# Kernel tuning notes

Hardware: AMD Instinct MI355X
Metric: run time of the kernel (lower is better)

## Reference

```python
import jax, jax.numpy as jnp
import numpy as np

B, N, D_M, H, D_K, R, GRID = 2, 2048, 128, 8, 16, 4, 64


def setup_inputs() -> dict:
    key = jax.random.key(0)
    ks = jax.random.split(key, 12)
    z = jax.random.normal(ks[0], (B, N, D_M), dtype=jnp.float32)
    patch_token = jax.random.normal(ks[1], (B, 1, D_M), dtype=jnp.float32)
    positions = jax.random.randint(ks[2], (B, N, 2), 0, GRID, dtype=jnp.int32)
    alive_mask = (jax.random.uniform(ks[3], (B, N, 1)) > 0.1).astype(jnp.float32)
    s = 0.02
    Wq = jax.random.normal(ks[4], (D_M, H * D_K), dtype=jnp.float32) * s
    Wk = jax.random.normal(ks[5], (D_M, H * D_K), dtype=jnp.float32) * s
    Wv = jax.random.normal(ks[6], (D_M, H * D_K), dtype=jnp.float32) * s
    Wo = jax.random.normal(ks[7], (H * D_K, D_M), dtype=jnp.float32) * s
    bq = jnp.zeros((H * D_K,), jnp.float32)
    bk = jnp.zeros((H * D_K,), jnp.float32)
    bv = jnp.zeros((H * D_K,), jnp.float32)
    bo = jnp.zeros((D_M,), jnp.float32)
    rel_bias = jax.random.normal(ks[8], (H, 2 * R + 1, 2 * R + 1), dtype=jnp.float32) * s
    return {"z": z, "patch_token": patch_token, "positions": positions, "alive_mask": alive_mask,
            "Wq": Wq, "bq": bq, "Wk": Wk, "bk": bk, "Wv": Wv, "bv": bv, "Wo": Wo, "bo": bo,
            "rel_bias": rel_bias}


def reference(z, patch_token, positions, alive_mask, Wq, bq, Wk, bk, Wv, bv, Wo, bo, rel_bias):
    B_, N_, _ = z.shape
    H_ = rel_bias.shape[0]
    R_ = (rel_bias.shape[1] - 1) // 2
    dk = Wq.shape[1] // H_
    alive = alive_mask                                   # [B,N,1] float 0/1
    z_a = z * alive
    tokens = jnp.concatenate([z_a, patch_token], axis=1)  # [B,N+1,d_m]
    q = (z_a @ Wq + bq).reshape(B_, N_, H_, dk).transpose(0, 2, 1, 3)       # [B,H,N,dk]
    k = (tokens @ Wk + bk).reshape(B_, N_ + 1, H_, dk).transpose(0, 2, 1, 3)
    v = (tokens @ Wv + bv).reshape(B_, N_ + 1, H_, dk).transpose(0, 2, 1, 3)
    q = q * alive[:, None]                               # [B,1,N,1] broadcast
    logits = jnp.einsum('bhnd,bhmd->bhnm', q, k) / jnp.sqrt(jnp.float32(dk))  # [B,H,N,N+1]
    # Chebyshev mask (delta = pos_i - pos_j)
    delta = positions[:, :, None, :] - positions[:, None, :, :]               # [B,N,N,2]
    cheb = jnp.maximum(jnp.abs(delta[..., 0]), jnp.abs(delta[..., 1]))
    alive_j = alive[:, :, 0] > 0
    not_self = ~jnp.eye(N_, dtype=bool)
    allowed = (cheb <= R_) & alive_j[:, None, :] & not_self[None]
    mask_agents = jnp.where(allowed, 0.0, -1e9).astype(jnp.float32)           # [B,N,N]
    # Relative-position bias (torch uses delta_rel = pos_j - pos_i = -delta)
    dx = -delta[..., 0] + R_
    dy = -delta[..., 1] + R_
    valid = (dx >= 0) & (dx <= 2 * R_) & (dy >= 0) & (dy <= 2 * R_)
    flat = jnp.clip(dx, 0, 2 * R_) * (2 * R_ + 1) + jnp.clip(dy, 0, 2 * R_)   # [B,N,N] int
    table = rel_bias.reshape(H_, -1)
    rel = jnp.moveaxis(jnp.take(table, flat, axis=1), 0, 1)                   # [B,H,N,N]
    rel = rel * valid[:, None].astype(jnp.float32)
    add = mask_agents[:, None] + rel                                          # [B,H,N,N]
    logits = logits + jnp.pad(add, ((0, 0), (0, 0), (0, 0), (0, 1)))          # patch col: mask 0, no bias
    logits = jnp.where(alive[:, None] > 0, logits, -1e9)                      # dead queries
    attn = jax.nn.softmax(logits, axis=-1)
    out = jnp.einsum('bhnm,bhmd->bhnd', attn, v)
    out = out.transpose(0, 2, 1, 3).reshape(B_, N_, H_ * dk)
    out = (out @ Wo + bo) * alive
    return out
```

## Files before the change

kernel.cpp:

```cpp
#include <hip/hip_runtime.h>
#include <hip/hip_fp16.h>
#include <math.h>

#define BB 2
#define NN 2048
#define NP1 2049
#define DM 128
#define NH 8
#define DK 16
#define RWIN 4
#define GRID_W 64
#define QPB 8
#define CAND_PQ 160

__device__ __forceinline__ void unpack8(uint4 r, float* f) {
    float2 t;
    t = __half22float2(*(const __half2*)&r.x); f[0] = t.x; f[1] = t.y;
    t = __half22float2(*(const __half2*)&r.y); f[2] = t.x; f[3] = t.y;
    t = __half22float2(*(const __half2*)&r.z); f[4] = t.x; f[5] = t.y;
    t = __half22float2(*(const __half2*)&r.w); f[6] = t.x; f[7] = t.y;
}


#define QKV_ROWS 8

__global__ __launch_bounds__(384) void qkv_kernel(
    const float* __restrict__ z, const float* __restrict__ patch,
    const float* __restrict__ Wq, const float* __restrict__ bq,
    const float* __restrict__ Wk, const float* __restrict__ bk,
    const float* __restrict__ Wv, const float* __restrict__ bv,
    float* __restrict__ q, __half* __restrict__ k, __half* __restrict__ v) {
    __shared__ float zrow[QKV_ROWS][DM];
    const int tid = threadIdx.x;
    const int mat = tid >> 7;
    const int rem = tid & 127;
    const int cg = rem & 31;
    const int rs = rem >> 5;
    const int r0 = blockIdx.x * QKV_ROWS;
    const int NROWS = BB * NP1;

    if (tid < QKV_ROWS * DM / 4) {
        int r = tid >> 5, q4 = tid & 31;
        int row = r0 + r;
        float4 val = make_float4(0.f, 0.f, 0.f, 0.f);
        if (row < NROWS) {
            int b = row / NP1, ti = row % NP1;
            const float* src = (ti < NN) ? (z + ((size_t)b * NN + ti) * DM)
                                         : (patch + (size_t)b * DM);
            val = ((const float4*)src)[q4];
        }
        *((float4*)&zrow[r][q4 * 4]) = val;
    }
    __syncthreads();

    const float* W    = (mat == 0) ? Wq : (mat == 1) ? Wk : Wv;
    const float* bias = (mat == 0) ? bq : (mat == 1) ? bk : bv;

    float a0x = 0.f, a0y = 0.f, a0z = 0.f, a0w = 0.f;
    float a1x = 0.f, a1y = 0.f, a1z = 0.f, a1w = 0.f;
#pragma unroll 8
    for (int kk = 0; kk < DM; ++kk) {
        float4 w4 = *((const float4*)(W + kk * DM + cg * 4));
        float z0 = zrow[rs][kk];
        float z1 = zrow[rs + 4][kk];
        a0x = fmaf(z0, w4.x, a0x); a0y = fmaf(z0, w4.y, a0y);
        a0z = fmaf(z0, w4.z, a0z); a0w = fmaf(z0, w4.w, a0w);
        a1x = fmaf(z1, w4.x, a1x); a1y = fmaf(z1, w4.y, a1y);
        a1z = fmaf(z1, w4.z, a1z); a1w = fmaf(z1, w4.w, a1w);
    }
    float4 b4 = *((const float4*)(bias + cg * 4));
    float4 o0 = make_float4(a0x + b4.x, a0y + b4.y, a0z + b4.z, a0w + b4.w);
    float4 o1 = make_float4(a1x + b4.x, a1y + b4.y, a1z + b4.z, a1w + b4.w);

#pragma unroll
    for (int rr = 0; rr < 2; ++rr) {
        int row = r0 + rs + rr * 4;
        if (row >= NROWS) break;
        float4 val = rr ? o1 : o0;
        int b = row / NP1, ti = row % NP1;
        if (mat == 0) {
            if (ti < NN) ((float4*)(q + ((size_t)b * NN + ti) * DM))[cg] = val;
        } else {
            __half2 p0 = __floats2half2_rn(val.x, val.y);
            __half2 p1 = __floats2half2_rn(val.z, val.w);
            uint2 st;
            st.x = *(unsigned int*)&p0;
            st.y = *(unsigned int*)&p1;
            __half* dst = ((mat == 1) ? k : v) + ((size_t)b * NP1 + ti) * DM;
            ((uint2*)dst)[cg] = st;
        }
    }
}


__global__ __launch_bounds__(256) void attn_out_kernel(
    const float* __restrict__ q, const __half* __restrict__ k, const __half* __restrict__ v,
    const int* __restrict__ positions, const float* __restrict__ alive,
    const float* __restrict__ rel_bias, const float* __restrict__ Wo,
    const float* __restrict__ bo, float* __restrict__ out) {
    const int tid = threadIdx.x;
    const int qq = tid >> 5;
    const int lane = tid & 31;
    const int h = lane >> 2;
    const int s = lane & 3;
    const int r0 = blockIdx.x * QPB;
    const int b = r0 >> 11;
    const int bi = r0 + qq;

    __shared__ float sbias[NH * 81];
    __shared__ int   spx[QPB], spy[QPB];
    __shared__ float sal[QPB];
    __shared__ int   mcount[QPB];
    __shared__ int   cand[QPB][CAND_PQ];
    __shared__ float po[QPB * 4][DM + 1];
    __shared__ float pl[QPB * 4][NH + 1];
    __shared__ float srow[QPB][DM + 1];

    if (tid < QPB) {
        mcount[tid] = 0;
        int gbi = r0 + tid;
        spx[tid] = positions[gbi * 2 + 0];
        spy[tid] = positions[gbi * 2 + 1];
        sal[tid] = alive[gbi];
    }
    for (int t = tid; t < NH * 81; t += 256) sbias[t] = rel_bias[t];

    const __half* kb = k + (size_t)b * NP1 * DM;
    const __half* vb = v + (size_t)b * NP1 * DM;

    float qf[16];
    {
        const float4* qr = (const float4*)(q + (size_t)bi * DM + h * DK);
#pragma unroll
        for (int e = 0; e < 4; ++e) {
            float4 t4 = qr[e];
            qf[e * 4 + 0] = t4.x * 0.25f; qf[e * 4 + 1] = t4.y * 0.25f;
            qf[e * 4 + 2] = t4.z * 0.25f; qf[e * 4 + 3] = t4.w * 0.25f;
        }
    }

    __syncthreads();

    int qx[QPB], qy[QPB], qi[QPB];
    float qa[QPB];
#pragma unroll
    for (int u = 0; u < QPB; ++u) {
        qx[u] = spx[u]; qy[u] = spy[u]; qa[u] = sal[u];
        qi[u] = (r0 + u) & (NN - 1);
    }

    const int2* pb = (const int2*)(positions + (size_t)b * NN * 2);
    const float* ab = alive + (size_t)b * NN;
#pragma unroll
    for (int u = 0; u < NN / 256; ++u) {
        int j = u * 256 + tid;
        int2 pj = pb[j];
        float aj = ab[j];
        if (aj > 0.5f) {
            int packed = j | (pj.x << 16) | (pj.y << 24);
#pragma unroll
            for (int qn = 0; qn < QPB; ++qn) {
                int dx = pj.x - qx[qn]; dx = dx < 0 ? -dx : dx;
                int dy = pj.y - qy[qn]; dy = dy < 0 ? -dy : dy;
                int ch = dx > dy ? dx : dy;
                if (ch <= RWIN && j != qi[qn] && qa[qn] > 0.5f) {
                    int slot = atomicAdd(&mcount[qn], 1);
                    if (slot < CAND_PQ) cand[qn][slot] = packed;
                }
            }
        }
    }
    __syncthreads();
    int M = mcount[qq]; if (M > CAND_PQ) M = CAND_PQ;
    const int pix = qx[qq], piy = qy[qq];

    float l = 0.f;
    float o[16];
#pragma unroll
    for (int e = 0; e < 16; ++e) o[e] = 0.f;

    if (s == 0) {
        const uint4* kr = (const uint4*)(kb + (size_t)NN * DM + h * DK);
        uint4 ka = kr[0], kb4 = kr[1];
        const uint4* vr = (const uint4*)(vb + (size_t)NN * DM + h * DK);
        uint4 va = vr[0], vb4 = vr[1];
        float kf[16], vf[16];
        unpack8(ka, kf); unpack8(kb4, kf + 8);
        unpack8(va, vf); unpack8(vb4, vf + 8);
        float d = 0.f;
#pragma unroll
        for (int e = 0; e < 16; ++e) d = fmaf(qf[e], kf[e], d);
        float p = __expf(d);
        l += p;
#pragma unroll
        for (int e = 0; e < 16; ++e) o[e] = fmaf(p, vf[e], o[e]);
    }

    for (int t = s; t < M; t += 4) {
        int packed = cand[qq][t];
        int j = packed & 0xFFFF;
        const uint4* kr = (const uint4*)(kb + (size_t)j * DM + h * DK);
        uint4 ka = kr[0], kb4 = kr[1];
        const uint4* vr = (const uint4*)(vb + (size_t)j * DM + h * DK);
        uint4 va = vr[0], vb4 = vr[1];
        float kf[16], vf[16];
        unpack8(ka, kf); unpack8(kb4, kf + 8);
        unpack8(va, vf); unpack8(vb4, vf + 8);
        float d = 0.f;
#pragma unroll
        for (int e = 0; e < 16; ++e) d = fmaf(qf[e], kf[e], d);
        int pjx = (packed >> 16) & 0xFF;
        int pjy = (packed >> 24) & 0xFF;
        float bias = sbias[h * 81 + (pjx - pix + RWIN) * 9 + (pjy - piy + RWIN)];
        float p = __expf(d + bias);
        l += p;
#pragma unroll
        for (int e = 0; e < 16; ++e) o[e] = fmaf(p, vf[e], o[e]);
    }

    {
        const int prow = qq * 4 + s;
#pragma unroll
        for (int e = 0; e < 16; ++e) po[prow][h * DK + e] = o[e];
        pl[prow][h] = l;
    }
    __syncthreads();
    {
        const int c = tid & 127;
        const int g = tid >> 7;
        const int ch = c >> 4;
#pragma unroll
        for (int qn = 0; qn < 4; ++qn) {
            int qq2 = g * 4 + qn;
            float acc = 0.f, lh = 0.f;
#pragma unroll
            for (int ss = 0; ss < 4; ++ss) {
                acc += po[qq2 * 4 + ss][c];
                lh  += pl[qq2 * 4 + ss][ch];
            }
            srow[qq2][c] = acc / lh;
        }
    }
    __syncthreads();

    {
        const int oq = tid >> 5;
        const int c4 = lane;
        float ax = 0.f, ay = 0.f, az = 0.f, aw = 0.f;
#pragma unroll 8
        for (int kk = 0; kk < DM; ++kk) {
            float sv = srow[oq][kk];
            float4 w4 = *((const float4*)(Wo + kk * DM + c4 * 4));
            ax = fmaf(sv, w4.x, ax); ay = fmaf(sv, w4.y, ay);
            az = fmaf(sv, w4.z, az); aw = fmaf(sv, w4.w, aw);
        }
        float ga = sal[oq] > 0.5f ? 1.f : 0.f;
        float4 b4 = *((const float4*)(bo + c4 * 4));
        float4 r;
        r.x = (ax + b4.x) * ga; r.y = (ay + b4.y) * ga;
        r.z = (az + b4.z) * ga; r.w = (aw + b4.w) * ga;
        ((float4*)(out + (size_t)(r0 + oq) * DM))[c4] = r;
    }
}

extern "C" void kernel_launch(void* const* d_in, const int* in_sizes, int n_in,
                              void* d_out, int out_size, void* d_ws, size_t ws_size,
                              hipStream_t stream) {
    const float* z         = (const float*)d_in[0];
    const float* patch     = (const float*)d_in[1];
    const int*   positions = (const int*)d_in[2];
    const float* alive     = (const float*)d_in[3];
    const float* Wq        = (const float*)d_in[4];
    const float* bq        = (const float*)d_in[5];
    const float* Wk        = (const float*)d_in[6];
    const float* bk        = (const float*)d_in[7];
    const float* Wv        = (const float*)d_in[8];
    const float* bv        = (const float*)d_in[9];
    const float* Wo        = (const float*)d_in[10];
    const float* bo        = (const float*)d_in[11];
    const float* rel_bias  = (const float*)d_in[12];
    float* out = (float*)d_out;

    char* ws = (char*)d_ws;
    size_t off = 0;
    auto alloc = [&](size_t bytes) -> void* {
        void* p = ws + off;
        off += (bytes + 255) & ~(size_t)255;
        return p;
    };
    float*  q = (float*)alloc((size_t)BB * NN * DM * 4);
    __half* k = (__half*)alloc((size_t)BB * NP1 * DM * 2);
    __half* v = (__half*)alloc((size_t)BB * NP1 * DM * 2);

    qkv_kernel<<<(BB * NP1 + QKV_ROWS - 1) / QKV_ROWS, 384, 0, stream>>>(z, patch, Wq, bq, Wk, bk, Wv, bv, q, k, v);
    attn_out_kernel<<<(BB * NN) / QPB, 256, 0, stream>>>(q, k, v, positions, alive, rel_bias, Wo, bo, out);
}
```

Before: 126.0 us.

## Fuse QKV projection and attention into one kernel with a grid-wide barrier

Merges the QKV projection kernel and the attention/output kernel into a single persistent launch of 512 blocks that synchronise through a global atomic counter barrier. The candidate-neighbour search runs before the barrier so it overlaps with other blocks finishing their projection tiles. This removes one kernel launch and the gap between kernels, but adds a hipMemsetAsync, a spin barrier that relies on all 512 blocks being co-resident, and a projection loop that now loads three weight matrices per thread.

```diff
diff --git a/kernel.cpp b/kernel.cpp
--- a/kernel.cpp
+++ b/kernel.cpp
@@ -12,6 +12,8 @@
 #define GRID_W 64
 #define QPB 8
 #define CAND_PQ 160
+#define NBLK 512
+#define NTILE 513
 
 __device__ __forceinline__ void unpack8(uint4 r, float* f) {
     float2 t;
@@ -22,91 +24,19 @@
 }
 
 
-#define QKV_ROWS 8
-
-__global__ __launch_bounds__(384) void qkv_kernel(
+__global__ __launch_bounds__(256, 2) void fused_kernel(
     const float* __restrict__ z, const float* __restrict__ patch,
     const float* __restrict__ Wq, const float* __restrict__ bq,
     const float* __restrict__ Wk, const float* __restrict__ bk,
     const float* __restrict__ Wv, const float* __restrict__ bv,
-    float* __restrict__ q, __half* __restrict__ k, __half* __restrict__ v) {
-    __shared__ float zrow[QKV_ROWS][DM];
-    const int tid = threadIdx.x;
-    const int mat = tid >> 7;
-    const int rem = tid & 127;
-    const int cg = rem & 31;
-    const int rs = rem >> 5;
-    const int r0 = blockIdx.x * QKV_ROWS;
-    const int NROWS = BB * NP1;
-
-    if (tid < QKV_ROWS * DM / 4) {
-        int r = tid >> 5, q4 = tid & 31;
-        int row = r0 + r;
-        float4 val = make_float4(0.f, 0.f, 0.f, 0.f);
-        if (row < NROWS) {
-            int b = row / NP1, ti = row % NP1;
-            const float* src = (ti < NN) ? (z + ((size_t)b * NN + ti) * DM)
-                                         : (patch + (size_t)b * DM);
-            val = ((const float4*)src)[q4];
-        }
-        *((float4*)&zrow[r][q4 * 4]) = val;
-    }
-    __syncthreads();
-
-    const float* W    = (mat == 0) ? Wq : (mat == 1) ? Wk : Wv;
-    const float* bias = (mat == 0) ? bq : (mat == 1) ? bk : bv;
-
-    float a0x = 0.f, a0y = 0.f, a0z = 0.f, a0w = 0.f;
-    float a1x = 0.f, a1y = 0.f, a1z = 0.f, a1w = 0.f;
-#pragma unroll 8
-    for (int kk = 0; kk < DM; ++kk) {
-        float4 w4 = *((const float4*)(W + kk * DM + cg * 4));
-        float z0 = zrow[rs][kk];
-        float z1 = zrow[rs + 4][kk];
-        a0x = fmaf(z0, w4.x, a0x); a0y = fmaf(z0, w4.y, a0y);
-        a0z = fmaf(z0, w4.z, a0z); a0w = fmaf(z0, w4.w, a0w);
-        a1x = fmaf(z1, w4.x, a1x); a1y = fmaf(z1, w4.y, a1y);
-        a1z = fmaf(z1, w4.z, a1z); a1w = fmaf(z1, w4.w, a1w);
-    }
-    float4 b4 = *((const float4*)(bias + cg * 4));
-    float4 o0 = make_float4(a0x + b4.x, a0y + b4.y, a0z + b4.z, a0w + b4.w);
-    float4 o1 = make_float4(a1x + b4.x, a1y + b4.y, a1z + b4.z, a1w + b4.w);
-
-#pragma unroll
-    for (int rr = 0; rr < 2; ++rr) {
-        int row = r0 + rs + rr * 4;
-        if (row >= NROWS) break;
-        float4 val = rr ? o1 : o0;
-        int b = row / NP1, ti = row % NP1;
-        if (mat == 0) {
-            if (ti < NN) ((float4*)(q + ((size_t)b * NN + ti) * DM))[cg] = val;
-        } else {
-            __half2 p0 = __floats2half2_rn(val.x, val.y);
-            __half2 p1 = __floats2half2_rn(val.z, val.w);
-            uint2 st;
-            st.x = *(unsigned int*)&p0;
-            st.y = *(unsigned int*)&p1;
-            __half* dst = ((mat == 1) ? k : v) + ((size_t)b * NP1 + ti) * DM;
-            ((uint2*)dst)[cg] = st;
-        }
-    }
-}
-
-
-__global__ __launch_bounds__(256) void attn_out_kernel(
-    const float* __restrict__ q, const __half* __restrict__ k, const __half* __restrict__ v,
     const int* __restrict__ positions, const float* __restrict__ alive,
     const float* __restrict__ rel_bias, const float* __restrict__ Wo,
-    const float* __restrict__ bo, float* __restrict__ out) {
+    const float* __restrict__ bo,
+    float* __restrict__ q, __half* __restrict__ k, __half* __restrict__ v,
+    int* __restrict__ bar, float* __restrict__ out) {
     const int tid = threadIdx.x;
-    const int qq = tid >> 5;
-    const int lane = tid & 31;
-    const int h = lane >> 2;
-    const int s = lane & 3;
-    const int r0 = blockIdx.x * QPB;
-    const int b = r0 >> 11;
-    const int bi = r0 + qq;
-
+
+    __shared__ float zrow[8][DM];
     __shared__ float sbias[NH * 81];
     __shared__ int   spx[QPB], spy[QPB];
     __shared__ float sal[QPB];
@@ -116,6 +46,70 @@
     __shared__ float pl[QPB * 4][NH + 1];
     __shared__ float srow[QPB][DM + 1];
 
+    {
+        const int cg = tid & 31;
+        const int rs = tid >> 5;
+        const int NROWS = BB * NP1;
+        for (int tile = blockIdx.x; tile < NTILE; tile += NBLK) {
+            __syncthreads();
+            {
+                int r = tid >> 5, c4 = tid & 31;
+                int row = tile * 8 + r;
+                float4 val = make_float4(0.f, 0.f, 0.f, 0.f);
+                if (row < NROWS) {
+                    int b = row / NP1, ti = row % NP1;
+                    const float* src = (ti < NN) ? (z + ((size_t)b * NN + ti) * DM)
+                                                 : (patch + (size_t)b * DM);
+                    val = ((const float4*)src)[c4];
+                }
+                *((float4*)&zrow[r][c4 * 4]) = val;
+            }
+            __syncthreads();
+            float aqx = 0.f, aqy = 0.f, aqz = 0.f, aqw = 0.f;
+            float akx = 0.f, aky = 0.f, akz = 0.f, akw = 0.f;
+            float avx = 0.f, avy = 0.f, avz = 0.f, avw = 0.f;
+#pragma unroll 4
+            for (int kk = 0; kk < DM; ++kk) {
+                float4 wq4 = *((const float4*)(Wq + kk * DM + cg * 4));
+                float4 wk4 = *((const float4*)(Wk + kk * DM + cg * 4));
+                float4 wv4 = *((const float4*)(Wv + kk * DM + cg * 4));
+                float z0 = zrow[rs][kk];
+                aqx = fmaf(z0, wq4.x, aqx); aqy = fmaf(z0, wq4.y, aqy);
+                aqz = fmaf(z0, wq4.z, aqz); aqw = fmaf(z0, wq4.w, aqw);
+                akx = fmaf(z0, wk4.x, akx); aky = fmaf(z0, wk4.y, aky);
+                akz = fmaf(z0, wk4.z, akz); akw = fmaf(z0, wk4.w, akw);
+                avx = fmaf(z0, wv4.x, avx); avy = fmaf(z0, wv4.y, avy);
+                avz = fmaf(z0, wv4.z, avz); avw = fmaf(z0, wv4.w, avw);
+            }
+            int row = tile * 8 + rs;
+            if (row < NROWS) {
+                int b = row / NP1, ti = row % NP1;
+                float4 bq4 = ((const float4*)bq)[cg];
+                float4 bk4 = ((const float4*)bk)[cg];
+                float4 bv4 = ((const float4*)bv)[cg];
+                if (ti < NN) {
+                    float4 oq = make_float4(aqx + bq4.x, aqy + bq4.y, aqz + bq4.z, aqw + bq4.w);
+                    ((float4*)(q + ((size_t)b * NN + ti) * DM))[cg] = oq;
+                }
+                {
+                    __half2 p0 = __floats2half2_rn(akx + bk4.x, aky + bk4.y);
+                    __half2 p1 = __floats2half2_rn(akz + bk4.z, akw + bk4.w);
+                    uint2 st; st.x = *(unsigned int*)&p0; st.y = *(unsigned int*)&p1;
+                    ((uint2*)(k + ((size_t)b * NP1 + ti) * DM))[cg] = st;
+                }
+                {
+                    __half2 p0 = __floats2half2_rn(avx + bv4.x, avy + bv4.y);
+                    __half2 p1 = __floats2half2_rn(avz + bv4.z, avw + bv4.w);
+                    uint2 st; st.x = *(unsigned int*)&p0; st.y = *(unsigned int*)&p1;
+                    ((uint2*)(v + ((size_t)b * NP1 + ti) * DM))[cg] = st;
+                }
+            }
+        }
+    }
+
+    const int r0 = blockIdx.x * QPB;
+    const int b = r0 >> 11;
+    __syncthreads();
     if (tid < QPB) {
         mcount[tid] = 0;
         int gbi = r0 + tid;
@@ -124,7 +118,53 @@
         sal[tid] = alive[gbi];
     }
     for (int t = tid; t < NH * 81; t += 256) sbias[t] = rel_bias[t];
-
+    __syncthreads();
+
+    int qx[QPB], qy[QPB], qi[QPB];
+    float qa[QPB];
+#pragma unroll
+    for (int u = 0; u < QPB; ++u) {
+        qx[u] = spx[u]; qy[u] = spy[u]; qa[u] = sal[u];
+        qi[u] = (r0 + u) & (NN - 1);
+    }
+    {
+        const int2* pb = (const int2*)(positions + (size_t)b * NN * 2);
+        const float* ab = alive + (size_t)b * NN;
+#pragma unroll
+        for (int u = 0; u < NN / 256; ++u) {
+            int j = u * 256 + tid;
+            int2 pj = pb[j];
+            float aj = ab[j];
+            if (aj > 0.5f) {
+                int packed = j | (pj.x << 16) | (pj.y << 24);
+#pragma unroll
+                for (int qn = 0; qn < QPB; ++qn) {
+                    int dx = pj.x - qx[qn]; dx = dx < 0 ? -dx : dx;
+                    int dy = pj.y - qy[qn]; dy = dy < 0 ? -dy : dy;
+                    int ch = dx > dy ? dx : dy;
+                    if (ch <= RWIN && j != qi[qn] && qa[qn] > 0.5f) {
+                        int slot = atomicAdd(&mcount[qn], 1);
+                        if (slot < CAND_PQ) cand[qn][slot] = packed;
+                    }
+                }
+            }
+        }
+    }
+
+    if (tid == 0) {
+        __threadfence();
+        atomicAdd(bar, 1);
+        while (__hip_atomic_load(bar, __ATOMIC_ACQUIRE, __HIP_MEMORY_SCOPE_AGENT) < NBLK) {
+            __builtin_amdgcn_s_sleep(2);
+        }
+    }
+    __syncthreads();
+
+    const int qq = tid >> 5;
+    const int lane = tid & 31;
+    const int h = lane >> 2;
+    const int s = lane & 3;
+    const int bi = r0 + qq;
     const __half* kb = k + (size_t)b * NP1 * DM;
     const __half* vb = v + (size_t)b * NP1 * DM;
 
@@ -138,40 +178,8 @@
             qf[e * 4 + 2] = t4.z * 0.25f; qf[e * 4 + 3] = t4.w * 0.25f;
         }
     }
-
-    __syncthreads();
-
-    int qx[QPB], qy[QPB], qi[QPB];
-    float qa[QPB];
-#pragma unroll
-    for (int u = 0; u < QPB; ++u) {
-        qx[u] = spx[u]; qy[u] = spy[u]; qa[u] = sal[u];
-        qi[u] = (r0 + u) & (NN - 1);
-    }
-
-    const int2* pb = (const int2*)(positions + (size_t)b * NN * 2);
-    const float* ab = alive + (size_t)b * NN;
-#pragma unroll
-    for (int u = 0; u < NN / 256; ++u) {
-        int j = u * 256 + tid;
-        int2 pj = pb[j];
-        float aj = ab[j];
-        if (aj > 0.5f) {
-            int packed = j | (pj.x << 16) | (pj.y << 24);
-#pragma unroll
-            for (int qn = 0; qn < QPB; ++qn) {
-                int dx = pj.x - qx[qn]; dx = dx < 0 ? -dx : dx;
-                int dy = pj.y - qy[qn]; dy = dy < 0 ? -dy : dy;
-                int ch = dx > dy ? dx : dy;
-                if (ch <= RWIN && j != qi[qn] && qa[qn] > 0.5f) {
-                    int slot = atomicAdd(&mcount[qn], 1);
-                    if (slot < CAND_PQ) cand[qn][slot] = packed;
-                }
-            }
-        }
-    }
-    __syncthreads();
     int M = mcount[qq]; if (M > CAND_PQ) M = CAND_PQ;
+    if (qa[qq] <= 0.5f) M = 0;
     const int pix = qx[qq], piy = qy[qq];
 
     float l = 0.f;
@@ -242,7 +250,6 @@
         }
     }
     __syncthreads();
-
     {
         const int oq = tid >> 5;
         const int c4 = lane;
@@ -288,10 +295,13 @@
         off += (bytes + 255) & ~(size_t)255;
         return p;
     };
-    float*  q = (float*)alloc((size_t)BB * NN * DM * 4);
-    __half* k = (__half*)alloc((size_t)BB * NP1 * DM * 2);
-    __half* v = (__half*)alloc((size_t)BB * NP1 * DM * 2);
-
-    qkv_kernel<<<(BB * NP1 + QKV_ROWS - 1) / QKV_ROWS, 384, 0, stream>>>(z, patch, Wq, bq, Wk, bk, Wv, bv, q, k, v);
-    attn_out_kernel<<<(BB * NN) / QPB, 256, 0, stream>>>(q, k, v, positions, alive, rel_bias, Wo, bo, out);
+    float*  q   = (float*)alloc((size_t)BB * NN * DM * 4);
+    __half* k   = (__half*)alloc((size_t)BB * NP1 * DM * 2);
+    __half* v   = (__half*)alloc((size_t)BB * NP1 * DM * 2);
+    int*    bar = (int*)alloc(256);
+
+    hipMemsetAsync(bar, 0, 8, stream);
+    fused_kernel<<<NBLK, 256, 0, stream>>>(z, patch, Wq, bq, Wk, bk, Wv, bv,
+                                           positions, alive, rel_bias, Wo, bo,
+                                           q, k, v, bar, out);
 }
```

New measurement: 194.4 us. +54.2%, slower.

## Fuse Q projection into attention kernel and enlarge KV projection tiles

Applied to the files above, without the earlier changes.

Q is no longer computed by the first kernel and stored to global memory. The attention kernel now loads its 8 z rows into shared memory and computes the scaled Q projection in place. The KV kernel handles 16 rows per block with 512 threads and only projects K and V. This removes the fp32 Q round-trip through global memory and shrinks the first kernel, at the cost of more shared memory and extra work per attention block, which could lower occupancy. Dead queries now get zero candidates explicitly.

```diff
diff --git a/kernel.cpp b/kernel.cpp
--- a/kernel.cpp
+++ b/kernel.cpp
@@ -22,39 +22,38 @@
 }
 
 
-#define QKV_ROWS 8
-
-__global__ __launch_bounds__(384) void qkv_kernel(
+#define KV_ROWS 16
+
+__global__ __launch_bounds__(512) void kv_kernel(
     const float* __restrict__ z, const float* __restrict__ patch,
-    const float* __restrict__ Wq, const float* __restrict__ bq,
     const float* __restrict__ Wk, const float* __restrict__ bk,
     const float* __restrict__ Wv, const float* __restrict__ bv,
-    float* __restrict__ q, __half* __restrict__ k, __half* __restrict__ v) {
-    __shared__ float zrow[QKV_ROWS][DM];
+    __half* __restrict__ k, __half* __restrict__ v) {
+    __shared__ float zrow[KV_ROWS][DM];
     const int tid = threadIdx.x;
-    const int mat = tid >> 7;
-    const int rem = tid & 127;
+    const int mat = tid >> 8;
+    const int rem = tid & 255;
     const int cg = rem & 31;
     const int rs = rem >> 5;
-    const int r0 = blockIdx.x * QKV_ROWS;
+    const int r0 = blockIdx.x * KV_ROWS;
     const int NROWS = BB * NP1;
 
-    if (tid < QKV_ROWS * DM / 4) {
-        int r = tid >> 5, q4 = tid & 31;
+    {
+        int r = tid >> 5, c4 = tid & 31;
         int row = r0 + r;
         float4 val = make_float4(0.f, 0.f, 0.f, 0.f);
         if (row < NROWS) {
             int b = row / NP1, ti = row % NP1;
             const float* src = (ti < NN) ? (z + ((size_t)b * NN + ti) * DM)
                                          : (patch + (size_t)b * DM);
-            val = ((const float4*)src)[q4];
-        }
-        *((float4*)&zrow[r][q4 * 4]) = val;
-    }
-    __syncthreads();
-
-    const float* W    = (mat == 0) ? Wq : (mat == 1) ? Wk : Wv;
-    const float* bias = (mat == 0) ? bq : (mat == 1) ? bk : bv;
+            val = ((const float4*)src)[c4];
+        }
+        *((float4*)&zrow[r][c4 * 4]) = val;
+    }
+    __syncthreads();
+
+    const float* W    = mat ? Wv : Wk;
+    const float* bias = mat ? bv : bk;
 
     float a0x = 0.f, a0y = 0.f, a0z = 0.f, a0w = 0.f;
     float a1x = 0.f, a1y = 0.f, a1z = 0.f, a1w = 0.f;
@@ -62,41 +61,36 @@
     for (int kk = 0; kk < DM; ++kk) {
         float4 w4 = *((const float4*)(W + kk * DM + cg * 4));
         float z0 = zrow[rs][kk];
-        float z1 = zrow[rs + 4][kk];
+        float z1 = zrow[rs + 8][kk];
         a0x = fmaf(z0, w4.x, a0x); a0y = fmaf(z0, w4.y, a0y);
         a0z = fmaf(z0, w4.z, a0z); a0w = fmaf(z0, w4.w, a0w);
         a1x = fmaf(z1, w4.x, a1x); a1y = fmaf(z1, w4.y, a1y);
         a1z = fmaf(z1, w4.z, a1z); a1w = fmaf(z1, w4.w, a1w);
     }
     float4 b4 = *((const float4*)(bias + cg * 4));
-    float4 o0 = make_float4(a0x + b4.x, a0y + b4.y, a0z + b4.z, a0w + b4.w);
-    float4 o1 = make_float4(a1x + b4.x, a1y + b4.y, a1z + b4.z, a1w + b4.w);
-
+    __half* dst = mat ? v : k;
 #pragma unroll
     for (int rr = 0; rr < 2; ++rr) {
-        int row = r0 + rs + rr * 4;
+        int row = r0 + rs + rr * 8;
         if (row >= NROWS) break;
-        float4 val = rr ? o1 : o0;
+        float rx = (rr ? a1x : a0x) + b4.x;
+        float ry = (rr ? a1y : a0y) + b4.y;
+        float rz = (rr ? a1z : a0z) + b4.z;
+        float rw = (rr ? a1w : a0w) + b4.w;
         int b = row / NP1, ti = row % NP1;
-        if (mat == 0) {
-            if (ti < NN) ((float4*)(q + ((size_t)b * NN + ti) * DM))[cg] = val;
-        } else {
-            __half2 p0 = __floats2half2_rn(val.x, val.y);
-            __half2 p1 = __floats2half2_rn(val.z, val.w);
-            uint2 st;
-            st.x = *(unsigned int*)&p0;
-            st.y = *(unsigned int*)&p1;
-            __half* dst = ((mat == 1) ? k : v) + ((size_t)b * NP1 + ti) * DM;
-            ((uint2*)dst)[cg] = st;
-        }
+        __half2 p0 = __floats2half2_rn(rx, ry);
+        __half2 p1 = __floats2half2_rn(rz, rw);
+        uint2 st; st.x = *(unsigned int*)&p0; st.y = *(unsigned int*)&p1;
+        ((uint2*)(dst + ((size_t)b * NP1 + ti) * DM))[cg] = st;
     }
 }
 
 
 __global__ __launch_bounds__(256) void attn_out_kernel(
-    const float* __restrict__ q, const __half* __restrict__ k, const __half* __restrict__ v,
+    const float* __restrict__ z, const __half* __restrict__ k, const __half* __restrict__ v,
     const int* __restrict__ positions, const float* __restrict__ alive,
-    const float* __restrict__ rel_bias, const float* __restrict__ Wo,
+    const float* __restrict__ rel_bias, const float* __restrict__ Wq,
+    const float* __restrict__ bq, const float* __restrict__ Wo,
     const float* __restrict__ bo, float* __restrict__ out) {
     const int tid = threadIdx.x;
     const int qq = tid >> 5;
@@ -105,13 +99,14 @@
     const int s = lane & 3;
     const int r0 = blockIdx.x * QPB;
     const int b = r0 >> 11;
-    const int bi = r0 + qq;
 
     __shared__ float sbias[NH * 81];
     __shared__ int   spx[QPB], spy[QPB];
     __shared__ float sal[QPB];
     __shared__ int   mcount[QPB];
     __shared__ int   cand[QPB][CAND_PQ];
+    __shared__ float zq[QPB][DM];
+    __shared__ float qrow[QPB][DM + 1];
     __shared__ float po[QPB * 4][DM + 1];
     __shared__ float pl[QPB * 4][NH + 1];
     __shared__ float srow[QPB][DM + 1];
@@ -124,22 +119,28 @@
         sal[tid] = alive[gbi];
     }
     for (int t = tid; t < NH * 81; t += 256) sbias[t] = rel_bias[t];
-
-    const __half* kb = k + (size_t)b * NP1 * DM;
-    const __half* vb = v + (size_t)b * NP1 * DM;
-
-    float qf[16];
-    {
-        const float4* qr = (const float4*)(q + (size_t)bi * DM + h * DK);
-#pragma unroll
-        for (int e = 0; e < 4; ++e) {
-            float4 t4 = qr[e];
-            qf[e * 4 + 0] = t4.x * 0.25f; qf[e * 4 + 1] = t4.y * 0.25f;
-            qf[e * 4 + 2] = t4.z * 0.25f; qf[e * 4 + 3] = t4.w * 0.25f;
-        }
-    }
-
-    __syncthreads();
+    {
+        int r = tid >> 5, c4 = tid & 31;
+        const float* src = z + ((size_t)b * NN + ((r0 + r) & (NN - 1))) * DM;
+        *((float4*)&zq[r][c4 * 4]) = ((const float4*)src)[c4];
+    }
+    __syncthreads();
+
+    {
+        float ax = 0.f, ay = 0.f, az = 0.f, aw = 0.f;
+#pragma unroll 8
+        for (int kk = 0; kk < DM; ++kk) {
+            float sv = zq[qq][kk];
+            float4 w4 = *((const float4*)(Wq + kk * DM + lane * 4));
+            ax = fmaf(sv, w4.x, ax); ay = fmaf(sv, w4.y, ay);
+            az = fmaf(sv, w4.z, az); aw = fmaf(sv, w4.w, aw);
+        }
+        float4 b4 = *((const float4*)(bq + lane * 4));
+        qrow[qq][lane * 4 + 0] = (ax + b4.x) * 0.25f;
+        qrow[qq][lane * 4 + 1] = (ay + b4.y) * 0.25f;
+        qrow[qq][lane * 4 + 2] = (az + b4.z) * 0.25f;
+        qrow[qq][lane * 4 + 3] = (aw + b4.w) * 0.25f;
+    }
 
     int qx[QPB], qy[QPB], qi[QPB];
     float qa[QPB];
@@ -149,29 +150,40 @@
         qi[u] = (r0 + u) & (NN - 1);
     }
 
-    const int2* pb = (const int2*)(positions + (size_t)b * NN * 2);
-    const float* ab = alive + (size_t)b * NN;
-#pragma unroll
-    for (int u = 0; u < NN / 256; ++u) {
-        int j = u * 256 + tid;
-        int2 pj = pb[j];
-        float aj = ab[j];
-        if (aj > 0.5f) {
-            int packed = j | (pj.x << 16) | (pj.y << 24);
-#pragma unroll
-            for (int qn = 0; qn < QPB; ++qn) {
-                int dx = pj.x - qx[qn]; dx = dx < 0 ? -dx : dx;
-                int dy = pj.y - qy[qn]; dy = dy < 0 ? -dy : dy;
-                int ch = dx > dy ? dx : dy;
-                if (ch <= RWIN && j != qi[qn] && qa[qn] > 0.5f) {
-                    int slot = atomicAdd(&mcount[qn], 1);
-                    if (slot < CAND_PQ) cand[qn][slot] = packed;
+    {
+        const int2* pb = (const int2*)(positions + (size_t)b * NN * 2);
+        const float* ab = alive + (size_t)b * NN;
+#pragma unroll
+        for (int u = 0; u < NN / 256; ++u) {
+            int j = u * 256 + tid;
+            int2 pj = pb[j];
+            float aj = ab[j];
+            if (aj > 0.5f) {
+                int packed = j | (pj.x << 16) | (pj.y << 24);
+#pragma unroll
+                for (int qn = 0; qn < QPB; ++qn) {
+                    int dx = pj.x - qx[qn]; dx = dx < 0 ? -dx : dx;
+                    int dy = pj.y - qy[qn]; dy = dy < 0 ? -dy : dy;
+                    int ch = dx > dy ? dx : dy;
+                    if (ch <= RWIN && j != qi[qn] && qa[qn] > 0.5f) {
+                        int slot = atomicAdd(&mcount[qn], 1);
+                        if (slot < CAND_PQ) cand[qn][slot] = packed;
+                    }
                 }
             }
         }
     }
     __syncthreads();
+
+    const __half* kb = k + (size_t)b * NP1 * DM;
+    const __half* vb = v + (size_t)b * NP1 * DM;
+
+    float qf[16];
+#pragma unroll
+    for (int e = 0; e < 16; ++e) qf[e] = qrow[qq][h * DK + e];
+
     int M = mcount[qq]; if (M > CAND_PQ) M = CAND_PQ;
+    if (qa[qq] <= 0.5f) M = 0;
     const int pix = qx[qq], piy = qy[qq];
 
     float l = 0.f;
@@ -245,21 +257,20 @@
 
     {
         const int oq = tid >> 5;
-        const int c4 = lane;
         float ax = 0.f, ay = 0.f, az = 0.f, aw = 0.f;
 #pragma unroll 8
         for (int kk = 0; kk < DM; ++kk) {
             float sv = srow[oq][kk];
-            float4 w4 = *((const float4*)(Wo + kk * DM + c4 * 4));
+            float4 w4 = *((const float4*)(Wo + kk * DM + lane * 4));
             ax = fmaf(sv, w4.x, ax); ay = fmaf(sv, w4.y, ay);
             az = fmaf(sv, w4.z, az); aw = fmaf(sv, w4.w, aw);
         }
         float ga = sal[oq] > 0.5f ? 1.f : 0.f;
-        float4 b4 = *((const float4*)(bo + c4 * 4));
+        float4 b4 = *((const float4*)(bo + lane * 4));
         float4 r;
         r.x = (ax + b4.x) * ga; r.y = (ay + b4.y) * ga;
         r.z = (az + b4.z) * ga; r.w = (aw + b4.w) * ga;
-        ((float4*)(out + (size_t)(r0 + oq) * DM))[c4] = r;
+        ((float4*)(out + (size_t)(r0 + oq) * DM))[lane] = r;
     }
 }
 
@@ -288,10 +299,9 @@
         off += (bytes + 255) & ~(size_t)255;
         return p;
     };
-    float*  q = (float*)alloc((size_t)BB * NN * DM * 4);
     __half* k = (__half*)alloc((size_t)BB * NP1 * DM * 2);
     __half* v = (__half*)alloc((size_t)BB * NP1 * DM * 2);
 
-    qkv_kernel<<<(BB * NP1 + QKV_ROWS - 1) / QKV_ROWS, 384, 0, stream>>>(z, patch, Wq, bq, Wk, bk, Wv, bv, q, k, v);
-    attn_out_kernel<<<(BB * NN) / QPB, 256, 0, stream>>>(q, k, v, positions, alive, rel_bias, Wo, bo, out);
+    kv_kernel<<<(BB * NP1 + KV_ROWS - 1) / KV_ROWS, 512, 0, stream>>>(z, patch, Wk, bk, Wv, bv, k, v);
+    attn_out_kernel<<<(BB * NN) / QPB, 256, 0, stream>>>(z, k, v, positions, alive, rel_bias, Wq, bq, Wo, bo, out);
 }
```

Result: slower. 131.3 us (+4.2%).

## Use 2 queries per block with 16-way candidate split per head

Applied to the files above, without the earlier changes.

Cuts queries per attention block from 8 to 2 and assigns 128 threads per query (16 lanes per head instead of 4) to walk the candidate list, so each block does a shorter serial walk and the grid has four times as many blocks. The reduction and output projection are rewritten to match, one thread per output column. In exchange, every block now rescans all 2048 positions to build candidates for only 2 queries, four times more total scan work, and it reads Wo four times as often.

```diff
diff --git a/kernel.cpp b/kernel.cpp
--- a/kernel.cpp
+++ b/kernel.cpp
@@ -10,7 +10,7 @@
 #define DK 16
 #define RWIN 4
 #define GRID_W 64
-#define QPB 8
+#define QPB 2
 #define CAND_PQ 160
 
 __device__ __forceinline__ void unpack8(uint4 r, float* f) {
@@ -99,10 +99,10 @@
     const float* __restrict__ rel_bias, const float* __restrict__ Wo,
     const float* __restrict__ bo, float* __restrict__ out) {
     const int tid = threadIdx.x;
-    const int qq = tid >> 5;
-    const int lane = tid & 31;
-    const int h = lane >> 2;
-    const int s = lane & 3;
+    const int qq = tid >> 7;
+    const int l7 = tid & 127;
+    const int h = l7 >> 4;
+    const int s = l7 & 15;
     const int r0 = blockIdx.x * QPB;
     const int b = r0 >> 11;
     const int bi = r0 + qq;
@@ -112,8 +112,8 @@
     __shared__ float sal[QPB];
     __shared__ int   mcount[QPB];
     __shared__ int   cand[QPB][CAND_PQ];
-    __shared__ float po[QPB * 4][DM + 1];
-    __shared__ float pl[QPB * 4][NH + 1];
+    __shared__ float po[QPB * 16][DM + 1];
+    __shared__ float pl[QPB * 16][NH + 1];
     __shared__ float srow[QPB][DM + 1];
 
     if (tid < QPB) {
@@ -149,23 +149,25 @@
         qi[u] = (r0 + u) & (NN - 1);
     }
 
-    const int2* pb = (const int2*)(positions + (size_t)b * NN * 2);
-    const float* ab = alive + (size_t)b * NN;
-#pragma unroll
-    for (int u = 0; u < NN / 256; ++u) {
-        int j = u * 256 + tid;
-        int2 pj = pb[j];
-        float aj = ab[j];
-        if (aj > 0.5f) {
-            int packed = j | (pj.x << 16) | (pj.y << 24);
-#pragma unroll
-            for (int qn = 0; qn < QPB; ++qn) {
-                int dx = pj.x - qx[qn]; dx = dx < 0 ? -dx : dx;
-                int dy = pj.y - qy[qn]; dy = dy < 0 ? -dy : dy;
-                int ch = dx > dy ? dx : dy;
-                if (ch <= RWIN && j != qi[qn] && qa[qn] > 0.5f) {
-                    int slot = atomicAdd(&mcount[qn], 1);
-                    if (slot < CAND_PQ) cand[qn][slot] = packed;
+    {
+        const int2* pb = (const int2*)(positions + (size_t)b * NN * 2);
+        const float* ab = alive + (size_t)b * NN;
+#pragma unroll
+        for (int u = 0; u < NN / 256; ++u) {
+            int j = u * 256 + tid;
+            int2 pj = pb[j];
+            float aj = ab[j];
+            if (aj > 0.5f) {
+                int packed = j | (pj.x << 16) | (pj.y << 24);
+#pragma unroll
+                for (int qn = 0; qn < QPB; ++qn) {
+                    int dx = pj.x - qx[qn]; dx = dx < 0 ? -dx : dx;
+                    int dy = pj.y - qy[qn]; dy = dy < 0 ? -dy : dy;
+                    int ch = dx > dy ? dx : dy;
+                    if (ch <= RWIN && j != qi[qn] && qa[qn] > 0.5f) {
+                        int slot = atomicAdd(&mcount[qn], 1);
+                        if (slot < CAND_PQ) cand[qn][slot] = packed;
+                    }
                 }
             }
         }
@@ -196,7 +198,7 @@
         for (int e = 0; e < 16; ++e) o[e] = fmaf(p, vf[e], o[e]);
     }
 
-    for (int t = s; t < M; t += 4) {
+    for (int t = s; t < M; t += 16) {
         int packed = cand[qq][t];
         int j = packed & 0xFFFF;
         const uint4* kr = (const uint4*)(kb + (size_t)j * DM + h * DK);
@@ -219,7 +221,7 @@
     }
 
     {
-        const int prow = qq * 4 + s;
+        const int prow = qq * 16 + s;
 #pragma unroll
         for (int e = 0; e < 16; ++e) po[prow][h * DK + e] = o[e];
         pl[prow][h] = l;
@@ -229,37 +231,25 @@
         const int c = tid & 127;
         const int g = tid >> 7;
         const int ch = c >> 4;
-#pragma unroll
-        for (int qn = 0; qn < 4; ++qn) {
-            int qq2 = g * 4 + qn;
-            float acc = 0.f, lh = 0.f;
-#pragma unroll
-            for (int ss = 0; ss < 4; ++ss) {
-                acc += po[qq2 * 4 + ss][c];
-                lh  += pl[qq2 * 4 + ss][ch];
-            }
-            srow[qq2][c] = acc / lh;
-        }
-    }
-    __syncthreads();
-
-    {
-        const int oq = tid >> 5;
-        const int c4 = lane;
-        float ax = 0.f, ay = 0.f, az = 0.f, aw = 0.f;
+        float acc = 0.f, lh = 0.f;
+#pragma unroll
+        for (int ss = 0; ss < 16; ++ss) {
+            acc += po[g * 16 + ss][c];
+            lh  += pl[g * 16 + ss][ch];
+        }
+        srow[g][c] = acc / lh;
+    }
+    __syncthreads();
+
+    {
+        const int oq = tid >> 7;
+        const int col = tid & 127;
+        float acc = 0.f;
 #pragma unroll 8
-        for (int kk = 0; kk < DM; ++kk) {
-            float sv = srow[oq][kk];
-            float4 w4 = *((const float4*)(Wo + kk * DM + c4 * 4));
-            ax = fmaf(sv, w4.x, ax); ay = fmaf(sv, w4.y, ay);
-            az = fmaf(sv, w4.z, az); aw = fmaf(sv, w4.w, aw);
-        }
+        for (int kk = 0; kk < DM; ++kk)
+            acc = fmaf(srow[oq][kk], Wo[kk * DM + col], acc);
         float ga = sal[oq] > 0.5f ? 1.f : 0.f;
-        float4 b4 = *((const float4*)(bo + c4 * 4));
-        float4 r;
-        r.x = (ax + b4.x) * ga; r.y = (ay + b4.y) * ga;
-        r.z = (az + b4.z) * ga; r.w = (aw + b4.w) * ga;
-        ((float4*)(out + (size_t)(r0 + oq) * DM))[c4] = r;
+        out[(size_t)(r0 + oq) * DM + col] = (acc + bo[col]) * ga;
     }
 }
 
```

Result: no change. 126.7 us (+0.5%).
